# Kernel optimization log

Measured on AMD Instinct MI355X. Metric: run time of the kernel, lower is better.

Reference implementation:

```python
import jax, jax.numpy as jnp
import numpy as np

D_MODEL = 512
N = 2048
BS = 8


def setup_inputs() -> dict:
    key = jax.random.key(0)
    ks = jax.random.split(key, 5)
    inputs1 = jax.random.normal(ks[0], (BS, N, D_MODEL), dtype=jnp.float32)
    inputs2 = jax.random.normal(ks[1], (BS, N, D_MODEL), dtype=jnp.float32)
    # torch Linear weights: init.normal_(std=0.001), bias=0
    Wq = 0.001 * jax.random.normal(ks[2], (D_MODEL, D_MODEL), dtype=jnp.float32)
    Wk = 0.001 * jax.random.normal(ks[3], (D_MODEL, D_MODEL), dtype=jnp.float32)
    Wv = 0.001 * jax.random.normal(ks[4], (D_MODEL, D_MODEL), dtype=jnp.float32)
    bq = jnp.zeros((D_MODEL,), dtype=jnp.float32)
    bk = jnp.zeros((D_MODEL,), dtype=jnp.float32)
    bv = jnp.zeros((D_MODEL,), dtype=jnp.float32)
    # nn.Parameter(torch.ones((n, n)))
    position_biases = jnp.ones((N, N), dtype=jnp.float32)
    return {"inputs1": inputs1, "inputs2": inputs2, "Wq": Wq, "bq": bq,
            "Wk": Wk, "bk": bk, "Wv": Wv, "bv": bv,
            "position_biases": position_biases}


def reference(inputs1, inputs2, Wq, bq, Wk, bk, Wv, bv, position_biases):
    # torch Linear: y = x @ W.T + b
    q = inputs1 @ Wq.T + bq                     # [b, n, d]
    k = inputs1 @ Wk.T + bk                     # [b, s, d]
    v = inputs2 @ Wv.T + bv                     # [b, s, d]
    # exp(k[b,s,d] + bias[t,s]) = exp(bias)[t,s] * exp(k)[b,s,d] -> separable,
    # avoiding the original's (n, bs, n, dim) broadcast intermediate.
    expB = jnp.exp(position_biases)             # [t, s]
    ek = jnp.exp(k)                             # [b, s, d]
    num = jnp.einsum('ts,bsd->btd', expB, ek * v)
    den = jnp.einsum('ts,bsd->btd', expB, ek)
    return jax.nn.sigmoid(q) * (num / den)      # [b, n, d]
```

## Files before the change

### kernel.cpp

```cpp
#include <hip/hip_runtime.h>

typedef float  f32x4  __attribute__((ext_vector_type(4)));
typedef __bf16 bf16x8 __attribute__((ext_vector_type(8)));
typedef __bf16 bf16x4 __attribute__((ext_vector_type(4)));

#define D_MODEL 512
#define SEQ     2048
#define BATCH   8
#define ROWS    (BATCH * SEQ)

#define ASYNC_COPY16(dst_lds, src_glb)                                          \
  __builtin_amdgcn_global_load_lds(                                             \
      (const __attribute__((address_space(1))) void*)(src_glb),                 \
      (__attribute__((address_space(3))) void*)(dst_lds), 16, 0, 0)

__global__ void cvt_all_kernel(const float* __restrict__ x1,
                               const float* __restrict__ x2,
                               const float* __restrict__ posb,
                               const float* __restrict__ Wq,
                               const float* __restrict__ Wk,
                               const float* __restrict__ Wv,
                               __bf16* __restrict__ x1b, __bf16* __restrict__ x2b,
                               __bf16* __restrict__ expBb, __bf16* __restrict__ wb)
{
  const int blk = blockIdx.x;
  if (blk < 16384) {
    const float* in = (blk < 8192) ? x1 : x2;
    __bf16* out = (blk < 8192) ? x1b : x2b;
    const int i = (blk & 8191) * 256 + threadIdx.x;
    float4 v = ((const float4*)in)[i];
    bf16x4 o = { (__bf16)v.x, (__bf16)v.y, (__bf16)v.z, (__bf16)v.w };
    ((bf16x4*)out)[i] = o;
  } else if (blk < 20480) {
    const int i = (blk - 16384) * 256 + threadIdx.x;
    float4 v = ((const float4*)posb)[i];
    bf16x4 o = { (__bf16)__expf(v.x), (__bf16)__expf(v.y),
                 (__bf16)__expf(v.z), (__bf16)__expf(v.w) };
    ((bf16x4*)expBb)[i] = o;
  } else {
    const int i = (blk - 20480) * 256 + threadIdx.x;
    const int nW4 = D_MODEL * D_MODEL / 4;
    const float* src = (i < nW4) ? Wq : (i < 2 * nW4) ? Wk : Wv;
    const int ii = i - ((i < nW4) ? 0 : (i < 2 * nW4) ? nW4 : 2 * nW4);
    float4 v = ((const float4*)src)[ii];
    bf16x4 o = { (__bf16)v.x, (__bf16)v.y, (__bf16)v.z, (__bf16)v.w };
    ((bf16x4*)wb)[i] = o;
  }
}

__global__ __launch_bounds__(512) void q_gemm_kernel(
    const __bf16* __restrict__ x1b, const __bf16* __restrict__ wb,
    const float* __restrict__ bq, __bf16* __restrict__ sigq)
{
  extern __shared__ __align__(16) __bf16 smem[];

  const int K = D_MODEL;
  const int tid  = threadIdx.x;
  const int wave = tid >> 6;
  const int lane = tid & 63;
  const int quad = lane >> 4;
  const int l16  = lane & 15;
  const int wm   = (wave >> 1) * 64;
  const int wn   = (wave & 1) * 64;
  const int m0   = blockIdx.x * 256;
  const int n0   = blockIdx.y * 128;
  const int l8r  = lane >> 3;
  const int scol = ((lane & 7) ^ l8r) * 8;

  const __bf16* ga[4]; const __bf16* gb[2];
  #pragma unroll
  for (int i = 0; i < 4; ++i)
    ga[i] = x1b + (long long)(m0 + i * 64 + wave * 8 + l8r) * K + scol;
  #pragma unroll
  for (int i = 0; i < 2; ++i)
    gb[i] = wb + (long long)(n0 + i * 64 + wave * 8 + l8r) * K + scol;

  f32x4 acc[4][4];
  #pragma unroll
  for (int i = 0; i < 4; ++i)
    #pragma unroll
    for (int j = 0; j < 4; ++j) acc[i][j] = (f32x4){0.f, 0.f, 0.f, 0.f};

  auto stageA2 = [&](int c, int k0, int i0) {
    ASYNC_COPY16(smem + c * 16384 + (i0 * 64 + wave * 8) * 64, ga[i0] + k0);
    ASYNC_COPY16(smem + c * 16384 + ((i0 + 1) * 64 + wave * 8) * 64, ga[i0 + 1] + k0);
  };
  auto stageB1 = [&](int c, int k0, int i) {
    ASYNC_COPY16(smem + 32768 + c * 8192 + (i * 64 + wave * 8) * 64, gb[i] + k0);
  };

  stageA2(0, 0, 0); stageA2(0, 0, 2);
  stageB1(0, 0, 0); stageB1(0, 0, 1);

  const int s0 = ((quad    ) ^ (l16 & 7)) * 8;
  const int s1 = ((quad + 4) ^ (l16 & 7)) * 8;

  for (int t = 0; t < 8; ++t) {
    const int c = t & 1;
    asm volatile("s_waitcnt vmcnt(0)" ::: "memory");
    __builtin_amdgcn_s_barrier();
    __builtin_amdgcn_sched_barrier(0);

    const __bf16* Ac = smem +         c * 16384 + (wm + l16) * 64;
    const __bf16* Bc = smem + 32768 + c * 8192  + (wn + l16) * 64;
    const bool pf = (t + 1 < 8);
    const int k1 = (t + 1) * 64;

    bf16x8 bfr[4][2];
    #pragma unroll
    for (int p = 0; p < 2; ++p) {
      if (p == 0) {
        #pragma unroll
        for (int j = 0; j < 4; ++j) {
          bfr[j][0] = *(const bf16x8*)&Bc[j * 1024 + s0];
          bfr[j][1] = *(const bf16x8*)&Bc[j * 1024 + s1];
        }
      }
      bf16x8 af[2][2];
      #pragma unroll
      for (int ii = 0; ii < 2; ++ii) {
        af[ii][0] = *(const bf16x8*)&Ac[(p * 2 + ii) * 1024 + s0];
        af[ii][1] = *(const bf16x8*)&Ac[(p * 2 + ii) * 1024 + s1];
      }
      if (pf) {
        if (p == 0) { stageA2(c ^ 1, k1, 0); stageB1(c ^ 1, k1, 0); }
        else        { stageA2(c ^ 1, k1, 2); stageB1(c ^ 1, k1, 1); }
      }
      __builtin_amdgcn_s_barrier();
      asm volatile("s_waitcnt lgkmcnt(0)" ::: "memory");
      __builtin_amdgcn_sched_barrier(0);
      __builtin_amdgcn_s_setprio(1);
      #pragma unroll
      for (int kk = 0; kk < 2; ++kk)
        #pragma unroll
        for (int ii = 0; ii < 2; ++ii)
          #pragma unroll
          for (int j = 0; j < 4; ++j)
            acc[p * 2 + ii][j] = __builtin_amdgcn_mfma_f32_16x16x32_bf16(
                af[ii][kk], bfr[j][kk], acc[p * 2 + ii][j], 0, 0, 0);
      __builtin_amdgcn_s_setprio(0);
      __builtin_amdgcn_s_barrier();
    }
  }

  #pragma unroll
  for (int j = 0; j < 4; ++j) {
    const int col = n0 + wn + j * 16 + l16;
    const float bvv = bq[col];
    #pragma unroll
    for (int i = 0; i < 4; ++i) {
      #pragma unroll
      for (int r = 0; r < 4; ++r) {
        const int row = m0 + wm + i * 16 + quad * 4 + r;
        float x = acc[i][j][r] + bvv;
        sigq[(long long)row * D_MODEL + col] = (__bf16)(1.f / (1.f + __expf(-x)));
      }
    }
  }
}

__global__ __launch_bounds__(512) void kv_fused_kernel(
    const __bf16* __restrict__ x1b, const __bf16* __restrict__ x2b,
    const __bf16* __restrict__ wb,
    const float* __restrict__ bk, const float* __restrict__ bv,
    __bf16* __restrict__ ekvT)
{
  extern __shared__ __align__(16) __bf16 smem[];

  const int K = D_MODEL;
  const int tid  = threadIdx.x;
  const int wave = tid >> 6;
  const int lane = tid & 63;
  const int quad = lane >> 4;
  const int l16  = lane & 15;
  const int wm   = (wave >> 1) * 64;
  const int wn   = (wave & 1) * 64;
  const int F0   = blockIdx.y * 256;
  const int L0   = blockIdx.x * 128;
  const int l8r  = lane >> 3;
  const int scol = ((lane & 7) ^ l8r) * 8;
  const bool hi  = (scol >= 32);
  const int sc   = scol & 31;

  const __bf16* Wkb = wb + (long long)D_MODEL * D_MODEL;
  const __bf16* Wvb = wb + 2LL * D_MODEL * D_MODEL;

  const __bf16* gW[4]; const __bf16* gX[2];
  #pragma unroll
  for (int i = 0; i < 4; ++i)
    gW[i] = (hi ? Wvb : Wkb) + (long long)(F0 + i * 64 + wave * 8 + l8r) * K + sc;
  #pragma unroll
  for (int i = 0; i < 2; ++i)
    gX[i] = (hi ? x2b : x1b) + (long long)(L0 + i * 64 + wave * 8 + l8r) * K + sc;

  f32x4 acck[4][4], accv[4][4];
  #pragma unroll
  for (int i = 0; i < 4; ++i)
    #pragma unroll
    for (int j = 0; j < 4; ++j) {
      acck[i][j] = (f32x4){0.f, 0.f, 0.f, 0.f};
      accv[i][j] = (f32x4){0.f, 0.f, 0.f, 0.f};
    }

  auto stageW = [&](int c, int k0) {
    #pragma unroll
    for (int i = 0; i < 4; ++i)
      ASYNC_COPY16(smem + c * 16384 + (i * 64 + wave * 8) * 64, gW[i] + k0);
  };
  auto stageX = [&](int c, int k0) {
    #pragma unroll
    for (int i = 0; i < 2; ++i)
      ASYNC_COPY16(smem + 32768 + c * 8192 + (i * 64 + wave * 8) * 64, gX[i] + k0);
  };

  stageW(0, 0); stageX(0, 0);

  const int s0 = ((quad    ) ^ (l16 & 7)) * 8;
  const int s1 = ((quad + 4) ^ (l16 & 7)) * 8;

  for (int s = 0; s < 16; ++s) {
    const int c = s & 1;
    asm volatile("s_waitcnt vmcnt(0)" ::: "memory");
    __builtin_amdgcn_s_barrier();
    __builtin_amdgcn_sched_barrier(0);

    const __bf16* Wc = smem +         c * 16384 + (wm + l16) * 64;
    const __bf16* Xc = smem + 32768 + c * 8192  + (wn + l16) * 64;
    const bool pf = (s + 1 < 16);
    const int k1 = (s + 1) * 32;

    {
      bf16x8 af[4], bfr[4];
      #pragma unroll
      for (int i = 0; i < 4; ++i) af[i]  = *(const bf16x8*)&Wc[i * 1024 + s0];
      #pragma unroll
      for (int j = 0; j < 4; ++j) bfr[j] = *(const bf16x8*)&Xc[j * 1024 + s0];
      if (pf) stageW(c ^ 1, k1);
      __builtin_amdgcn_s_barrier();
      asm volatile("s_waitcnt lgkmcnt(0)" ::: "memory");
      __builtin_amdgcn_sched_barrier(0);
      __builtin_amdgcn_s_setprio(1);
      #pragma unroll
      for (int i = 0; i < 4; ++i)
        #pragma unroll
        for (int j = 0; j < 4; ++j)
          acck[i][j] = __builtin_amdgcn_mfma_f32_16x16x32_bf16(
              af[i], bfr[j], acck[i][j], 0, 0, 0);
      __builtin_amdgcn_s_setprio(0);
      __builtin_amdgcn_s_barrier();
    }
    {
      bf16x8 af[4], bfr[4];
      #pragma unroll
      for (int i = 0; i < 4; ++i) af[i]  = *(const bf16x8*)&Wc[i * 1024 + s1];
      #pragma unroll
      for (int j = 0; j < 4; ++j) bfr[j] = *(const bf16x8*)&Xc[j * 1024 + s1];
      if (pf) stageX(c ^ 1, k1);
      __builtin_amdgcn_s_barrier();
      asm volatile("s_waitcnt lgkmcnt(0)" ::: "memory");
      __builtin_amdgcn_sched_barrier(0);
      __builtin_amdgcn_s_setprio(1);
      #pragma unroll
      for (int i = 0; i < 4; ++i)
        #pragma unroll
        for (int j = 0; j < 4; ++j)
          accv[i][j] = __builtin_amdgcn_mfma_f32_16x16x32_bf16(
              af[i], bfr[j], accv[i][j], 0, 0, 0);
      __builtin_amdgcn_s_setprio(0);
      __builtin_amdgcn_s_barrier();
    }
  }

  const int b   = L0 >> 11;
  const int sb  = L0 & 2047;
  __bf16* outb = ekvT + (long long)b * (2 * D_MODEL) * SEQ + sb;
  #pragma unroll
  for (int i = 0; i < 4; ++i) {
    #pragma unroll
    for (int r = 0; r < 4; ++r) {
      const int d = F0 + wm + i * 16 + quad * 4 + r;
      const float bkd = bk[d];
      const float bvd = bv[d];
      const int gr = ((d >> 5) << 6) + (d & 31);
      #pragma unroll
      for (int j = 0; j < 4; ++j) {
        const int ss = wn + j * 16 + l16;
        const float kkv = acck[i][j][r] + bkd;
        const float vvv = accv[i][j][r] + bvd;
        const float ekf = __expf(kkv);
        outb[(long long)gr * SEQ + ss]        = (__bf16)(ekf * vvv);
        outb[(long long)(gr + 32) * SEQ + ss] = (__bf16)ekf;
      }
    }
  }
}

#define ENT32 (SEQ / 32)

__global__ __launch_bounds__(512) void einsum_fused_kernel(
    const __bf16* __restrict__ A, const __bf16* __restrict__ BtAll,
    const __bf16* __restrict__ sigq, float* __restrict__ out)
{
  extern __shared__ __align__(16) __bf16 smem[];

  const int b = blockIdx.z;
  const __bf16* Bt = BtAll + (long long)b * (2 * D_MODEL) * SEQ;

  const int tid  = threadIdx.x;
  const int wave = tid >> 6;
  const int lane = tid & 63;
  const int quad = lane >> 4;
  const int l16  = lane & 15;
  const int wm   = (wave >> 2) * 128;
  const int wn   = (wave & 3) * 64;
  const int m0   = blockIdx.x * 256;
  const int n0   = blockIdx.y * 256;

  const int qr = (tid >> 2) ^ ((tid >> 4) & 1);
  const int cs = (((tid & 3) ^ (qr & 3))) * 8;
  const __bf16* gA0 = A  + (long long)(m0 +       qr) * SEQ + cs;
  const __bf16* gA1 = A  + (long long)(m0 + 128 + qr) * SEQ + cs;
  const __bf16* gB0 = Bt + (long long)(n0 +       qr) * SEQ + cs;
  const __bf16* gB1 = Bt + (long long)(n0 + 128 + qr) * SEQ + cs;

  const int lxb = l16 ^ ((l16 >> 2) & 1);
  const int sl  = (quad ^ (l16 & 3)) * 8;

  f32x4 acc[8][4];
  #pragma unroll
  for (int i = 0; i < 8; ++i)
    #pragma unroll
    for (int j = 0; j < 4; ++j) acc[i][j] = (f32x4){0.f, 0.f, 0.f, 0.f};

  auto stage = [&](int t) {
    const int c  = t & 3;
    const int k0 = t * 32;
    ASYNC_COPY16(smem +         c * 8192 +        tid * 8, gA0 + k0);
    ASYNC_COPY16(smem +         c * 8192 + 4096 + tid * 8, gA1 + k0);
    ASYNC_COPY16(smem + 32768 + c * 8192 +        tid * 8, gB0 + k0);
    ASYNC_COPY16(smem + 32768 + c * 8192 + 4096 + tid * 8, gB1 + k0);
  };

  stage(0); stage(1); stage(2);

  for (int t = 0; t < ENT32; ++t) {
    const int c = t & 3;
    if (t < ENT32 - 2)
      asm volatile("s_waitcnt vmcnt(8) lgkmcnt(0)" ::: "memory");
    else if (t == ENT32 - 2)
      asm volatile("s_waitcnt vmcnt(4) lgkmcnt(0)" ::: "memory");
    else
      asm volatile("s_waitcnt vmcnt(0) lgkmcnt(0)" ::: "memory");
    __builtin_amdgcn_s_barrier();
    __builtin_amdgcn_sched_barrier(0);

    const __bf16* Ac = smem +         c * 8192 + (wm + lxb) * 32 + sl;
    const __bf16* Bc = smem + 32768 + c * 8192 + (wn + lxb) * 32 + sl;

    bf16x8 af[8], bfr[4];
    #pragma unroll
    for (int i = 0; i < 8; ++i) af[i]  = *(const bf16x8*)&Ac[i * 512];
    #pragma unroll
    for (int j = 0; j < 4; ++j) bfr[j] = *(const bf16x8*)&Bc[j * 512];

    if (t + 3 < ENT32) stage(t + 3);

    #pragma unroll
    for (int i = 0; i < 8; ++i)
      #pragma unroll
      for (int j = 0; j < 4; ++j)
        acc[i][j] = __builtin_amdgcn_mfma_f32_16x16x32_bf16(
            af[i], bfr[j], acc[i][j], 0, 0, 0);
  }

  const int g = (n0 + wn) >> 6;
  #pragma unroll
  for (int j = 0; j < 2; ++j) {
    const int d = g * 32 + j * 16 + l16;
    #pragma unroll
    for (int i = 0; i < 8; ++i) {
      #pragma unroll
      for (int r = 0; r < 4; ++r) {
        const int row = m0 + wm + i * 16 + quad * 4 + r;
        const long long off = ((long long)b * SEQ + row) * D_MODEL + d;
        const float num = acc[i][j][r];
        const float den = acc[i][j + 2][r];
        out[off] = (float)sigq[off] * (num / den);
      }
    }
  }
}

extern "C" void kernel_launch(void* const* d_in, const int* in_sizes, int n_in,
                              void* d_out, int out_size, void* d_ws, size_t ws_size,
                              hipStream_t stream) {
  const float* inputs1 = (const float*)d_in[0];
  const float* inputs2 = (const float*)d_in[1];
  const float* Wq = (const float*)d_in[2];
  const float* bq = (const float*)d_in[3];
  const float* Wk = (const float*)d_in[4];
  const float* bk = (const float*)d_in[5];
  const float* Wv = (const float*)d_in[6];
  const float* bv = (const float*)d_in[7];
  const float* posb = (const float*)d_in[8];
  float* out = (float*)d_out;

  char* ws = (char*)d_ws;
  const long long szX  = (long long)ROWS * D_MODEL * 2;
  const long long szW  = (long long)D_MODEL * D_MODEL * 2;
  const long long szEB = (long long)SEQ * SEQ * 2;
  const long long szT  = (long long)BATCH * 2 * D_MODEL * SEQ * 2;
  __bf16* x1b   = (__bf16*)(ws);                 ws += szX;
  __bf16* x2b   = (__bf16*)(ws);                 ws += szX;
  __bf16* wb    = (__bf16*)(ws);                 ws += 3 * szW;
  __bf16* expBb = (__bf16*)(ws);                 ws += szEB;
  __bf16* sigq  = (__bf16*)(ws);                 ws += szX;
  __bf16* ekvT  = (__bf16*)(ws);                 ws += szT;

  static bool attr_done = false;
  if (!attr_done) {
    hipFuncSetAttribute((const void*)einsum_fused_kernel,
                        hipFuncAttributeMaxDynamicSharedMemorySize, 131072);
    hipFuncSetAttribute((const void*)q_gemm_kernel,
                        hipFuncAttributeMaxDynamicSharedMemorySize, 98304);
    hipFuncSetAttribute((const void*)kv_fused_kernel,
                        hipFuncAttributeMaxDynamicSharedMemorySize, 98304);
    attr_done = true;
  }

  cvt_all_kernel<<<21248, 256, 0, stream>>>(inputs1, inputs2, posb,
                                            Wq, Wk, Wv,
                                            x1b, x2b, expBb, wb);

  {
    dim3 g(ROWS / 256, D_MODEL / 128);
    q_gemm_kernel<<<g, 512, 98304, stream>>>(x1b, wb, bq, sigq);
  }

  {
    dim3 g(ROWS / 128, D_MODEL / 256);
    kv_fused_kernel<<<g, 512, 98304, stream>>>(x1b, x2b, wb, bk, bv, ekvT);
  }

  {
    dim3 g(SEQ / 256, (2 * D_MODEL) / 256, BATCH);
    einsum_fused_kernel<<<g, 512, 131072, stream>>>(expBb, ekvT, sigq, out);
  }
}
```

Baseline: 242.8 us.

## Remap block order for L2 locality and use XOR-swizzled paired-row LDS layout

Remaps the linear block index so that consecutive workgroups share the same column tile and batch, with the row tile varying fastest, aiming to improve L2/MALL reuse of the B operand. The global-to-LDS copy layout changes to pack two 32-element rows per 64-element LDS line with an 8-way XOR swizzle, and the fragment read offsets change to match, aiming to reduce LDS bank conflicts on the ds_read_b128 loads. This risks layout mismatches between the write and read indexing, and the remap assumes a fixed 8x4x8 grid shape.

```diff
diff --git a/kernel.cpp b/kernel.cpp
--- a/kernel.cpp
+++ b/kernel.cpp
@@ -303,9 +303,6 @@
 {
   extern __shared__ __align__(16) __bf16 smem[];
 
-  const int b = blockIdx.z;
-  const __bf16* Bt = BtAll + (long long)b * (2 * D_MODEL) * SEQ;
-
   const int tid  = threadIdx.x;
   const int wave = tid >> 6;
   const int lane = tid & 63;
@@ -313,18 +310,28 @@
   const int l16  = lane & 15;
   const int wm   = (wave >> 2) * 128;
   const int wn   = (wave & 3) * 64;
-  const int m0   = blockIdx.x * 256;
-  const int n0   = blockIdx.y * 256;
-
-  const int qr = (tid >> 2) ^ ((tid >> 4) & 1);
-  const int cs = (((tid & 3) ^ (qr & 3))) * 8;
-  const __bf16* gA0 = A  + (long long)(m0 +       qr) * SEQ + cs;
-  const __bf16* gA1 = A  + (long long)(m0 + 128 + qr) * SEQ + cs;
-  const __bf16* gB0 = Bt + (long long)(n0 +       qr) * SEQ + cs;
-  const __bf16* gB1 = Bt + (long long)(n0 + 128 + qr) * SEQ + cs;
-
-  const int lxb = l16 ^ ((l16 >> 2) & 1);
-  const int sl  = (quad ^ (l16 & 3)) * 8;
+
+  const int lid  = blockIdx.x + (blockIdx.y << 3) + (blockIdx.z << 5);
+  const int orig = ((lid & 7) << 5) + (lid >> 3);
+  const int m0   = (orig & 7) * 256;
+  const int n0   = ((orig >> 3) & 3) * 256;
+  const int b    = orig >> 5;
+
+  const __bf16* Bt = BtAll + (long long)b * (2 * D_MODEL) * SEQ;
+
+  const int pr = tid >> 3;
+  const int u  = (tid & 7) ^ (pr & 7);
+  const int lr = 2 * pr + (u >> 2);
+  const int cs = (u & 3) * 8;
+  const __bf16* gA0 = A  + (long long)(m0 +       lr) * SEQ + cs;
+  const __bf16* gA1 = A  + (long long)(m0 + 128 + lr) * SEQ + cs;
+  const __bf16* gB0 = Bt + (long long)(n0 +       lr) * SEQ + cs;
+  const __bf16* gB1 = Bt + (long long)(n0 + 128 + lr) * SEQ + cs;
+
+  const int rl   = l16 >> 1;
+  const int gran = (((l16 & 1) << 2) | quad) ^ rl;
+  const int offA = (wave >> 2) * 4096 + rl * 64 + gran * 8;
+  const int offB = (wn >> 7) * 4096 + ((wn & 127) >> 1) * 64 + rl * 64 + gran * 8;
 
   f32x4 acc[8][4];
   #pragma unroll
@@ -354,8 +361,8 @@
     __builtin_amdgcn_s_barrier();
     __builtin_amdgcn_sched_barrier(0);
 
-    const __bf16* Ac = smem +         c * 8192 + (wm + lxb) * 32 + sl;
-    const __bf16* Bc = smem + 32768 + c * 8192 + (wn + lxb) * 32 + sl;
+    const __bf16* Ac = smem +         c * 8192 + offA;
+    const __bf16* Bc = smem + 32768 + c * 8192 + offB;
 
     bf16x8 af[8], bfr[4];
     #pragma unroll
```

New measurement: 238.1 us. No clear change (-1.9%).
